# Kernel tuning notes

Measured on AMD Instinct MI355X. Metric: run time of the kernel, lower is better.

The kernel has to match this reference:

```python
import jax, jax.numpy as jnp
import numpy as np

N_NODES = 100000
N_EDGES = 1000000
IN_FEATS = 128
HID = 128
OUT_FEATS = 64


def _glorot(key, shape):
    fan_in, fan_out = shape
    lim = (6.0 / (fan_in + fan_out)) ** 0.5
    return jax.random.uniform(key, shape, jnp.float32, -lim, lim)


def setup_inputs() -> dict:
    key = jax.random.key(0)
    ks = jax.random.split(key, 12)
    x = jax.random.normal(ks[0], (N_NODES, IN_FEATS), jnp.float32)
    src = jax.random.randint(ks[1], (N_EDGES,), 0, N_NODES, jnp.int32)
    dst = jax.random.randint(ks[2], (N_EDGES,), 0, N_NODES, jnp.int32)
    return {
        "x": x, "src": src, "dst": dst,
        "w_self0": _glorot(ks[3], (IN_FEATS, HID)),
        "w_neigh0": _glorot(ks[4], (IN_FEATS, HID)),
        "b0": jnp.zeros((HID,), jnp.float32),
        "w_self1": _glorot(ks[5], (HID, HID)),
        "w_neigh1": _glorot(ks[6], (HID, HID)),
        "b1": jnp.zeros((HID,), jnp.float32),
        "w_self2": _glorot(ks[7], (HID, OUT_FEATS)),
        "w_neigh2": _glorot(ks[8], (HID, OUT_FEATS)),
        "b2": jnp.zeros((OUT_FEATS,), jnp.float32),
    }


def _sage_conv(x, src, dst, deg_inv, w_self, w_neigh, b):
    # irregular gather over neighbors, then mean segment-reduce onto dst
    neigh_sum = jax.ops.segment_sum(x[src], dst, num_segments=x.shape[0])  # [N, d]
    neigh_mean = neigh_sum * deg_inv  # zero-in-degree nodes -> 0
    return x @ w_self + neigh_mean @ w_neigh + b


def reference(x, src, dst,
              w_self0, w_neigh0, b0,
              w_self1, w_neigh1, b1,
              w_self2, w_neigh2, b2):
    n = x.shape[0]
    deg = jax.ops.segment_sum(jnp.ones_like(dst, jnp.float32), dst, num_segments=n)
    deg_inv = jnp.where(deg > 0, 1.0 / jnp.maximum(deg, 1.0), 0.0)[:, None]  # [N,1]
    h = _sage_conv(x, src, dst, deg_inv, w_self0, w_neigh0, b0)
    h = jax.nn.relu(h)  # dropout is identity in eval
    h = _sage_conv(h, src, dst, deg_inv, w_self1, w_neigh1, b1)
    h = jax.nn.relu(h)
    h = _sage_conv(h, src, dst, deg_inv, w_self2, w_neigh2, b2)
    return h
```

## Files before the change

kernel.cpp:

```cpp
#include <hip/hip_runtime.h>
#include <stdint.h>

#define N_NODES 100000
#define N_EDGES 1000000
#define NB 782
#define CAP 4096
#define EPB 2048
#define SCB ((N_EDGES + EPB - 1) / EPB)
#define PREPB 6442

typedef __attribute__((ext_vector_type(2))) _Float16 f16x2;
typedef __attribute__((ext_vector_type(8))) _Float16 f16x8;
typedef __attribute__((ext_vector_type(4))) float f32x4;

__device__ __forceinline__ unsigned short f2h(float f) {
  _Float16 h = (_Float16)f;
  return *(unsigned short*)&h;
}

__global__ void k_scatter_prep(const int* __restrict__ src, const int* __restrict__ dst,
                               int* __restrict__ bcnt, unsigned int* __restrict__ stage,
                               const float* __restrict__ x, unsigned short* __restrict__ xb,
                               const float* __restrict__ ws0, const float* __restrict__ wn0,
                               unsigned short* __restrict__ wt0,
                               const float* __restrict__ ws1, const float* __restrict__ wn1,
                               unsigned short* __restrict__ wt1,
                               const float* __restrict__ ws2, const float* __restrict__ wn2,
                               unsigned short* __restrict__ wt2) {
  __shared__ int h[NB];
  __shared__ int cur[NB];
  int t = threadIdx.x;
  if (blockIdx.x < SCB) {
    for (int i = t; i < NB; i += 256) h[i] = 0;
    __syncthreads();
    int base = blockIdx.x * EPB;
#pragma unroll 8
    for (int k = 0; k < EPB / 256; k++) {
      int i = base + t + k * 256;
      if (i < N_EDGES) atomicAdd(&h[dst[i] >> 7], 1);
    }
    __syncthreads();
    for (int i = t; i < NB; i += 256) {
      int c = h[i];
      cur[i] = c ? atomicAdd(&bcnt[i], c) : 0;
    }
    __syncthreads();
#pragma unroll 8
    for (int k = 0; k < EPB / 256; k++) {
      int i = base + t + k * 256;
      if (i < N_EDGES) {
        int d = dst[i];
        int b = d >> 7;
        int pos = atomicAdd(&cur[b], 1);
        stage[(size_t)b * CAP + pos] = ((unsigned int)(d & 127) << 17) | (unsigned int)src[i];
      }
    }
    return;
  }
  int b = blockIdx.x - SCB;
  if (b < 6250) {
    int i = b * 256 + t;
    float4 a = ((const float4*)x)[2 * i];
    float4 v = ((const float4*)x)[2 * i + 1];
    unsigned short r[8] = {f2h(a.x), f2h(a.y), f2h(a.z), f2h(a.w),
                           f2h(v.x), f2h(v.y), f2h(v.z), f2h(v.w)};
    *(uint4*)(xb + (size_t)i * 8) = *(uint4*)r;
    return;
  }
  int w = (b - 6250) * 256 + t;
  if (w < 16384) {
    int n = w >> 7, k = w & 127;
    wt0[n * 256 + k] = f2h(ws0[(size_t)k * 128 + n]);
    wt0[n * 256 + 128 + k] = f2h(wn0[(size_t)k * 128 + n]);
  } else if (w < 32768) {
    w -= 16384;
    int n = w >> 7, k = w & 127;
    wt1[n * 256 + k] = f2h(ws1[(size_t)k * 128 + n]);
    wt1[n * 256 + 128 + k] = f2h(wn1[(size_t)k * 128 + n]);
  } else {
    w -= 32768;
    int n = w >> 7, k = w & 127;
    float v = (n < 64) ? ws2[(size_t)k * 64 + n] : wn2[(size_t)k * 64 + (n - 64)];
    wt2[n * 128 + k] = f2h(v);
  }
}

__global__ void k_bucket(const unsigned int* __restrict__ stage, const int* __restrict__ bcnt,
                         int* __restrict__ csr, int* __restrict__ rowbeg,
                         int* __restrict__ rowend, float* __restrict__ dinv) {
  __shared__ int cnt[128], sc[128], cur[128];
  int b = blockIdx.x, t = threadIdx.x;
  int nb = bcnt[b];
  const unsigned int* sb = stage + (size_t)b * CAP;
  int e0 = b * CAP;
  if (t < 128) cnt[t] = 0;
  __syncthreads();
  for (int e = t; e < nb; e += 256)
    atomicAdd(&cnt[sb[e] >> 17], 1);
  __syncthreads();
  int myc = (t < 128) ? cnt[t] : 0;
  if (t < 128) sc[t] = myc;
  __syncthreads();
  for (int off = 1; off < 128; off <<= 1) {
    int a = (t < 128 && t >= off) ? sc[t - off] : 0;
    __syncthreads();
    if (t < 128) sc[t] += a;
    __syncthreads();
  }
  if (t < 128) {
    int node = b * 128 + t;
    int ex = sc[t] - myc;
    cur[t] = ex;
    if (node < N_NODES) {
      rowbeg[node] = e0 + ex;
      rowend[node] = e0 + ex + myc;
      dinv[node] = myc ? 1.0f / (float)myc : 0.0f;
    }
  }
  __syncthreads();
  for (int e = t; e < nb; e += 256) {
    unsigned int v = sb[e];
    int l = v >> 17;
    int pos = e0 + atomicAdd(&cur[l], 1);
    csr[pos] = (int)(v & 0x1FFFFu);
  }
}

__global__ void k_agg(const unsigned short* __restrict__ feat,
                      const int* __restrict__ rowbeg, const int* __restrict__ rowend,
                      const int* __restrict__ csr,
                      const float* __restrict__ dinv, unsigned short* __restrict__ nm) {
  int wv = threadIdx.x >> 6, lane = threadIdx.x & 63;
  int node = blockIdx.x * 4 + wv;
  if (node >= N_NODES) return;
  const uint4* fp = (const uint4*)feat;
  int s0 = rowbeg[node], s1 = rowend[node];
  int g = lane >> 4, c = lane & 15;
  f16x2 q0 = {0, 0}, q1 = {0, 0}, q2 = {0, 0}, q3 = {0, 0};
  for (int j = s0 + g; j < s1; j += 16) {
    int i1 = j + 4, i2 = j + 8, i3 = j + 12;
    bool h1 = i1 < s1, h2 = i2 < s1, h3 = i3 < s1;
    int c0 = csr[j];
    int c1 = h1 ? csr[i1] : 0;
    int c2 = h2 ? csr[i2] : 0;
    int c3 = h3 ? csr[i3] : 0;
    uint4 v0, v1, v2, v3;
    v0 = fp[(size_t)c0 * 16 + c];
    if (h1) v1 = fp[(size_t)c1 * 16 + c];
    if (h2) v2 = fp[(size_t)c2 * 16 + c];
    if (h3) v3 = fp[(size_t)c3 * 16 + c];
    q0 += *(const f16x2*)&v0.x; q1 += *(const f16x2*)&v0.y;
    q2 += *(const f16x2*)&v0.z; q3 += *(const f16x2*)&v0.w;
    if (h1) {
      q0 += *(const f16x2*)&v1.x; q1 += *(const f16x2*)&v1.y;
      q2 += *(const f16x2*)&v1.z; q3 += *(const f16x2*)&v1.w;
    }
    if (h2) {
      q0 += *(const f16x2*)&v2.x; q1 += *(const f16x2*)&v2.y;
      q2 += *(const f16x2*)&v2.z; q3 += *(const f16x2*)&v2.w;
    }
    if (h3) {
      q0 += *(const f16x2*)&v3.x; q1 += *(const f16x2*)&v3.y;
      q2 += *(const f16x2*)&v3.z; q3 += *(const f16x2*)&v3.w;
    }
  }
  float a0 = (float)q0[0], a1 = (float)q0[1], a2 = (float)q1[0], a3 = (float)q1[1];
  float a4 = (float)q2[0], a5 = (float)q2[1], a6 = (float)q3[0], a7 = (float)q3[1];
#define RED(x) x += __shfl_xor(x, 16); x += __shfl_xor(x, 32);
  RED(a0) RED(a1) RED(a2) RED(a3) RED(a4) RED(a5) RED(a6) RED(a7)
#undef RED
  if (g == 0) {
    float di = dinv[node];
    uint4 o;
    o.x = ((unsigned int)f2h(a1 * di) << 16) | (unsigned int)f2h(a0 * di);
    o.y = ((unsigned int)f2h(a3 * di) << 16) | (unsigned int)f2h(a2 * di);
    o.z = ((unsigned int)f2h(a5 * di) << 16) | (unsigned int)f2h(a4 * di);
    o.w = ((unsigned int)f2h(a7 * di) << 16) | (unsigned int)f2h(a6 * di);
    ((uint4*)(nm + (size_t)node * 128))[c] = o;
  }
}

__global__ void k_agg2(const unsigned short* __restrict__ zn,
                       const int* __restrict__ rowbeg, const int* __restrict__ rowend,
                       const int* __restrict__ csr, const float* __restrict__ dinv,
                       const float* __restrict__ self2, float* __restrict__ out) {
  int wv = threadIdx.x >> 6, lane = threadIdx.x & 63;
  int node = blockIdx.x * 4 + wv;
  if (node >= N_NODES) return;
  const uint4* fp = (const uint4*)zn;
  int s0 = rowbeg[node], s1 = rowend[node];
  int g = lane >> 3, c = lane & 7;
  f16x2 q0 = {0, 0}, q1 = {0, 0}, q2 = {0, 0}, q3 = {0, 0};
  for (int j = s0 + g; j < s1; j += 32) {
    int i1 = j + 8, i2 = j + 16, i3 = j + 24;
    bool h1 = i1 < s1, h2 = i2 < s1, h3 = i3 < s1;
    int c0 = csr[j];
    int c1 = h1 ? csr[i1] : 0;
    int c2 = h2 ? csr[i2] : 0;
    int c3 = h3 ? csr[i3] : 0;
    uint4 v0, v1, v2, v3;
    v0 = fp[(size_t)c0 * 8 + c];
    if (h1) v1 = fp[(size_t)c1 * 8 + c];
    if (h2) v2 = fp[(size_t)c2 * 8 + c];
    if (h3) v3 = fp[(size_t)c3 * 8 + c];
    q0 += *(const f16x2*)&v0.x; q1 += *(const f16x2*)&v0.y;
    q2 += *(const f16x2*)&v0.z; q3 += *(const f16x2*)&v0.w;
    if (h1) {
      q0 += *(const f16x2*)&v1.x; q1 += *(const f16x2*)&v1.y;
      q2 += *(const f16x2*)&v1.z; q3 += *(const f16x2*)&v1.w;
    }
    if (h2) {
      q0 += *(const f16x2*)&v2.x; q1 += *(const f16x2*)&v2.y;
      q2 += *(const f16x2*)&v2.z; q3 += *(const f16x2*)&v2.w;
    }
    if (h3) {
      q0 += *(const f16x2*)&v3.x; q1 += *(const f16x2*)&v3.y;
      q2 += *(const f16x2*)&v3.z; q3 += *(const f16x2*)&v3.w;
    }
  }
  float a0 = (float)q0[0], a1 = (float)q0[1], a2 = (float)q1[0], a3 = (float)q1[1];
  float a4 = (float)q2[0], a5 = (float)q2[1], a6 = (float)q3[0], a7 = (float)q3[1];
#define RED8(x) x += __shfl_xor(x, 8); x += __shfl_xor(x, 16); x += __shfl_xor(x, 32);
  RED8(a0) RED8(a1) RED8(a2) RED8(a3) RED8(a4) RED8(a5) RED8(a6) RED8(a7)
#undef RED8
  if (g == 0) {
    float di = dinv[node];
    const float4* sp = (const float4*)(self2 + (size_t)node * 64);
    float4 s0v = sp[c * 2], s1v = sp[c * 2 + 1];
    float4 o0 = {s0v.x + a0 * di, s0v.y + a1 * di, s0v.z + a2 * di, s0v.w + a3 * di};
    float4 o1 = {s1v.x + a4 * di, s1v.y + a5 * di, s1v.z + a6 * di, s1v.w + a7 * di};
    float4* op = (float4*)(out + (size_t)node * 64);
    op[c * 2] = o0;
    op[c * 2 + 1] = o1;
  }
}

template <int NOUT, bool RELU>
__global__ __launch_bounds__(256, 4) void k_mm(
    const unsigned short* __restrict__ A0, const unsigned short* __restrict__ A1,
    const unsigned short* __restrict__ WT, const float* __restrict__ Bv,
    unsigned short* __restrict__ OUT) {
  constexpr int NFC = NOUT / 64;
  __shared__ __align__(16) unsigned short sm[16896];
  const int row0 = blockIdx.x * 64;
  const int tid = threadIdx.x;

  for (int i = tid; i < 1024; i += 256) {
    int r = i >> 4, c = i & 15;
    int gr = row0 + r;
    if (gr >= N_NODES) gr = N_NODES - 1;
    *(uint4*)(sm + r * 264 + c * 8) = ((const uint4*)(A0 + (size_t)gr * 128))[c];
    *(uint4*)(sm + r * 264 + 128 + c * 8) = ((const uint4*)(A1 + (size_t)gr * 128))[c];
  }

  const int lane = tid & 63;
  const int w = tid >> 6;
  const int r16 = lane & 15;
  const int kg = lane >> 4;
  const int wc0 = w * (NOUT / 4);

  f32x4 acc[4][NFC];
#pragma unroll
  for (int rf = 0; rf < 4; rf++)
#pragma unroll
    for (int cf = 0; cf < NFC; cf++) acc[rf][cf] = (f32x4){0.f, 0.f, 0.f, 0.f};

  __syncthreads();

  const unsigned short* wtb = WT + (size_t)(wc0 + r16) * 256 + kg * 8;
  const unsigned short* asb = sm + r16 * 264 + kg * 8;

  for (int ks = 0; ks < 8; ks++) {
    f16x8 a[4];
#pragma unroll
    for (int rf = 0; rf < 4; rf++)
      a[rf] = *(const f16x8*)(asb + rf * 16 * 264 + ks * 32);
#pragma unroll
    for (int cf = 0; cf < NFC; cf++) {
      f16x8 b = *(const f16x8*)(wtb + cf * 16 * 256 + ks * 32);
#pragma unroll
      for (int rf = 0; rf < 4; rf++)
        acc[rf][cf] = __builtin_amdgcn_mfma_f32_16x16x32_f16(a[rf], b, acc[rf][cf], 0, 0, 0);
    }
  }

  __syncthreads();

  constexpr int LSO = NOUT + 8;
  unsigned short* so = sm;
#pragma unroll
  for (int rf = 0; rf < 4; rf++)
#pragma unroll
    for (int cf = 0; cf < NFC; cf++) {
      int col = wc0 + cf * 16 + r16;
      float bias = Bv[col];
#pragma unroll
      for (int r = 0; r < 4; r++) {
        int row = rf * 16 + kg * 4 + r;
        float v = acc[rf][cf][r] + bias;
        if (RELU) v = fmaxf(v, 0.f);
        so[row * LSO + col] = f2h(v);
      }
    }
  __syncthreads();
  for (int i = tid; i < 64 * (NOUT / 8); i += 256) {
    int r = i / (NOUT / 8), c = i % (NOUT / 8);
    int gr = row0 + r;
    if (gr < N_NODES)
      *(uint4*)(OUT + (size_t)gr * NOUT + c * 8) = *(const uint4*)(so + r * LSO + c * 8);
  }
}

__global__ __launch_bounds__(256, 4) void k_mm2(
    const unsigned short* __restrict__ A, const unsigned short* __restrict__ WT,
    const float* __restrict__ Bv, float* __restrict__ SELF,
    unsigned short* __restrict__ ZN) {
  __shared__ __align__(16) unsigned short sm[64 * 136];
  const int row0 = blockIdx.x * 64;
  const int tid = threadIdx.x;

  for (int i = tid; i < 1024; i += 256) {
    int r = i >> 4, c = i & 15;
    int gr = row0 + r;
    if (gr >= N_NODES) gr = N_NODES - 1;
    *(uint4*)(sm + r * 136 + c * 8) = ((const uint4*)(A + (size_t)gr * 128))[c];
  }

  const int lane = tid & 63;
  const int w = tid >> 6;
  const int r16 = lane & 15;
  const int kg = lane >> 4;
  const int wc0 = w * 32;

  f32x4 acc[4][2];
#pragma unroll
  for (int rf = 0; rf < 4; rf++)
#pragma unroll
    for (int cf = 0; cf < 2; cf++) acc[rf][cf] = (f32x4){0.f, 0.f, 0.f, 0.f};

  __syncthreads();

  const unsigned short* wtb = WT + (size_t)(wc0 + r16) * 128 + kg * 8;
  const unsigned short* asb = sm + r16 * 136 + kg * 8;

  for (int ks = 0; ks < 4; ks++) {
    f16x8 a[4];
#pragma unroll
    for (int rf = 0; rf < 4; rf++)
      a[rf] = *(const f16x8*)(asb + rf * 16 * 136 + ks * 32);
#pragma unroll
    for (int cf = 0; cf < 2; cf++) {
      f16x8 b = *(const f16x8*)(wtb + cf * 16 * 128 + ks * 32);
#pragma unroll
      for (int rf = 0; rf < 4; rf++)
        acc[rf][cf] = __builtin_amdgcn_mfma_f32_16x16x32_f16(a[rf], b, acc[rf][cf], 0, 0, 0);
    }
  }

  __syncthreads();

  float* sof = (float*)sm;
#pragma unroll
  for (int rf = 0; rf < 4; rf++)
#pragma unroll
    for (int cf = 0; cf < 2; cf++) {
      int col = wc0 + cf * 16 + r16;
      if (col < 64) {
        float bias = Bv[col];
#pragma unroll
        for (int r = 0; r < 4; r++) {
          int row = rf * 16 + kg * 4 + r;
          sof[row * 68 + col] = acc[rf][cf][r] + bias;
        }
      }
    }
  __syncthreads();
  for (int i = tid; i < 1024; i += 256) {
    int r = i >> 4, c = i & 15;
    int gr = row0 + r;
    if (gr < N_NODES)
      *(float4*)(SELF + (size_t)gr * 64 + c * 4) = *(const float4*)(sof + r * 68 + c * 4);
  }
  __syncthreads();

  unsigned short* soh = sm;
#pragma unroll
  for (int rf = 0; rf < 4; rf++)
#pragma unroll
    for (int cf = 0; cf < 2; cf++) {
      int col = wc0 + cf * 16 + r16;
      if (col >= 64) {
#pragma unroll
        for (int r = 0; r < 4; r++) {
          int row = rf * 16 + kg * 4 + r;
          soh[row * 72 + (col - 64)] = f2h(acc[rf][cf][r]);
        }
      }
    }
  __syncthreads();
  for (int i = tid; i < 512; i += 256) {
    int r = i >> 3, c = i & 7;
    int gr = row0 + r;
    if (gr < N_NODES)
      *(uint4*)(ZN + (size_t)gr * 64 + c * 8) = *(const uint4*)(soh + r * 72 + c * 8);
  }
}


extern "C" void kernel_launch(void* const* d_in, const int* in_sizes, int n_in,
                              void* d_out, int out_size, void* d_ws, size_t ws_size,
                              hipStream_t stream) {
  const float* x   = (const float*)d_in[0];
  const int*   src = (const int*)d_in[1];
  const int*   dst = (const int*)d_in[2];
  const float* ws0 = (const float*)d_in[3];
  const float* wn0 = (const float*)d_in[4];
  const float* b0  = (const float*)d_in[5];
  const float* ws1 = (const float*)d_in[6];
  const float* wn1 = (const float*)d_in[7];
  const float* b1  = (const float*)d_in[8];
  const float* ws2 = (const float*)d_in[9];
  const float* wn2 = (const float*)d_in[10];
  const float* b2  = (const float*)d_in[11];
  float* out = (float*)d_out;

  uint8_t* base = (uint8_t*)d_ws;
  size_t off = 0;
  auto alloc = [&](size_t bytes) -> void* {
    void* p = base + off;
    off = (off + bytes + 255) & ~(size_t)255;
    return p;
  };
  int*   rowbeg  = (int*)alloc((size_t)N_NODES * 4);
  int*   rowend  = (int*)alloc((size_t)N_NODES * 4);
  float* dinv    = (float*)alloc((size_t)N_NODES * 4);
  int*   csr     = (int*)alloc((size_t)NB * CAP * 4);
  unsigned int* stage = (unsigned int*)alloc((size_t)NB * CAP * 4);
  int*   bcnt    = (int*)alloc((size_t)NB * 4);
  unsigned short* xb  = (unsigned short*)alloc((size_t)N_NODES * 128 * 2);
  unsigned short* nmb = (unsigned short*)alloc((size_t)N_NODES * 128 * 2);
  unsigned short* h1b = (unsigned short*)alloc((size_t)N_NODES * 128 * 2);
  unsigned short* h2b = (unsigned short*)alloc((size_t)N_NODES * 128 * 2);
  float* self2 = (float*)alloc((size_t)N_NODES * 64 * 4);
  unsigned short* znb = (unsigned short*)alloc((size_t)N_NODES * 64 * 2);
  unsigned short* wt0 = (unsigned short*)alloc(128 * 256 * 2);
  unsigned short* wt1 = (unsigned short*)alloc(128 * 256 * 2);
  unsigned short* wt2 = (unsigned short*)alloc(128 * 128 * 2);

  hipMemsetAsync(bcnt, 0, (size_t)NB * 4, stream);
  k_scatter_prep<<<SCB + PREPB, 256, 0, stream>>>(src, dst, bcnt, stage,
                                                  x, xb, ws0, wn0, wt0,
                                                  ws1, wn1, wt1, ws2, wn2, wt2);
  k_bucket<<<NB, 256, 0, stream>>>(stage, bcnt, csr, rowbeg, rowend, dinv);

  const int GMM = (N_NODES + 63) / 64;

  k_agg<<<25000, 256, 0, stream>>>(xb, rowbeg, rowend, csr, dinv, nmb);
  k_mm<128, true><<<GMM, 256, 0, stream>>>(xb, nmb, wt0, b0, h1b);
  k_agg<<<25000, 256, 0, stream>>>(h1b, rowbeg, rowend, csr, dinv, nmb);
  k_mm<128, true><<<GMM, 256, 0, stream>>>(h1b, nmb, wt1, b1, h2b);
  k_mm2<<<GMM, 256, 0, stream>>>(h2b, wt2, b2, self2, znb);
  k_agg2<<<25000, 256, 0, stream>>>(znb, rowbeg, rowend, csr, dinv, self2, out);
}
```

Baseline: 238.5 us.

## Replace global-atomic bucket scatter with count/scan/scatter passes and enlarge aggregation blocks

```diff
diff --git a/kernel.cpp b/kernel.cpp
--- a/kernel.cpp
+++ b/kernel.cpp
@@ -4,7 +4,7 @@
 #define N_NODES 100000
 #define N_EDGES 1000000
 #define NB 782
-#define CAP 4096
+#define CAP 2048
 #define EPB 2048
 #define SCB ((N_EDGES + EPB - 1) / EPB)
 #define PREPB 6442
@@ -18,17 +18,15 @@
   return *(unsigned short*)&h;
 }
 
-__global__ void k_scatter_prep(const int* __restrict__ src, const int* __restrict__ dst,
-                               int* __restrict__ bcnt, unsigned int* __restrict__ stage,
-                               const float* __restrict__ x, unsigned short* __restrict__ xb,
-                               const float* __restrict__ ws0, const float* __restrict__ wn0,
-                               unsigned short* __restrict__ wt0,
-                               const float* __restrict__ ws1, const float* __restrict__ wn1,
-                               unsigned short* __restrict__ wt1,
-                               const float* __restrict__ ws2, const float* __restrict__ wn2,
-                               unsigned short* __restrict__ wt2) {
+__global__ void k_count_prep(const int* __restrict__ dst, int* __restrict__ hcnt,
+                             const float* __restrict__ x, unsigned short* __restrict__ xb,
+                             const float* __restrict__ ws0, const float* __restrict__ wn0,
+                             unsigned short* __restrict__ wt0,
+                             const float* __restrict__ ws1, const float* __restrict__ wn1,
+                             unsigned short* __restrict__ wt1,
+                             const float* __restrict__ ws2, const float* __restrict__ wn2,
+                             unsigned short* __restrict__ wt2) {
   __shared__ int h[NB];
-  __shared__ int cur[NB];
   int t = threadIdx.x;
   if (blockIdx.x < SCB) {
     for (int i = t; i < NB; i += 256) h[i] = 0;
@@ -40,21 +38,8 @@
       if (i < N_EDGES) atomicAdd(&h[dst[i] >> 7], 1);
     }
     __syncthreads();
-    for (int i = t; i < NB; i += 256) {
-      int c = h[i];
-      cur[i] = c ? atomicAdd(&bcnt[i], c) : 0;
-    }
-    __syncthreads();
-#pragma unroll 8
-    for (int k = 0; k < EPB / 256; k++) {
-      int i = base + t + k * 256;
-      if (i < N_EDGES) {
-        int d = dst[i];
-        int b = d >> 7;
-        int pos = atomicAdd(&cur[b], 1);
-        stage[(size_t)b * CAP + pos] = ((unsigned int)(d & 127) << 17) | (unsigned int)src[i];
-      }
-    }
+    int* hrow = hcnt + (size_t)blockIdx.x * NB;
+    for (int i = t; i < NB; i += 256) hrow[i] = h[i];
     return;
   }
   int b = blockIdx.x - SCB;
@@ -85,6 +70,44 @@
   }
 }
 
+__global__ __launch_bounds__(512) void k_hscan(const int* __restrict__ hcnt,
+                                               int* __restrict__ hoff,
+                                               int* __restrict__ bcnt) {
+  __shared__ int sc[512];
+  int bucket = blockIdx.x, t = threadIdx.x;
+  int v = (t < SCB) ? hcnt[(size_t)t * NB + bucket] : 0;
+  sc[t] = v;
+  __syncthreads();
+  for (int off = 1; off < 512; off <<= 1) {
+    int a = (t >= off) ? sc[t - off] : 0;
+    __syncthreads();
+    sc[t] += a;
+    __syncthreads();
+  }
+  hoff[(size_t)bucket * 512 + t] = sc[t] - v;
+  if (t == 511) bcnt[bucket] = sc[511];
+}
+
+__global__ void k_scatter(const int* __restrict__ src, const int* __restrict__ dst,
+                          const int* __restrict__ hoff, unsigned int* __restrict__ stage) {
+  __shared__ int cur[NB];
+  int t = threadIdx.x;
+  int blk = blockIdx.x;
+  for (int i = t; i < NB; i += 256) cur[i] = hoff[(size_t)i * 512 + blk];
+  __syncthreads();
+  int base = blk * EPB;
+#pragma unroll 8
+  for (int k = 0; k < EPB / 256; k++) {
+    int i = base + t + k * 256;
+    if (i < N_EDGES) {
+      int d = dst[i];
+      int b = d >> 7;
+      int pos = atomicAdd(&cur[b], 1);
+      stage[(size_t)b * CAP + pos] = ((unsigned int)(d & 127) << 17) | (unsigned int)src[i];
+    }
+  }
+}
+
 __global__ void k_bucket(const unsigned int* __restrict__ stage, const int* __restrict__ bcnt,
                          int* __restrict__ csr, int* __restrict__ rowbeg,
                          int* __restrict__ rowend, float* __restrict__ dinv) {
@@ -126,12 +149,13 @@
   }
 }
 
-__global__ void k_agg(const unsigned short* __restrict__ feat,
-                      const int* __restrict__ rowbeg, const int* __restrict__ rowend,
-                      const int* __restrict__ csr,
-                      const float* __restrict__ dinv, unsigned short* __restrict__ nm) {
+__global__ __launch_bounds__(1024) void k_agg(
+    const unsigned short* __restrict__ feat,
+    const int* __restrict__ rowbeg, const int* __restrict__ rowend,
+    const int* __restrict__ csr,
+    const float* __restrict__ dinv, unsigned short* __restrict__ nm) {
   int wv = threadIdx.x >> 6, lane = threadIdx.x & 63;
-  int node = blockIdx.x * 4 + wv;
+  int node = blockIdx.x * 16 + wv;
   if (node >= N_NODES) return;
   const uint4* fp = (const uint4*)feat;
   int s0 = rowbeg[node], s1 = rowend[node];
@@ -180,12 +204,13 @@
   }
 }
 
-__global__ void k_agg2(const unsigned short* __restrict__ zn,
-                       const int* __restrict__ rowbeg, const int* __restrict__ rowend,
-                       const int* __restrict__ csr, const float* __restrict__ dinv,
-                       const float* __restrict__ self2, float* __restrict__ out) {
+__global__ __launch_bounds__(1024) void k_agg2(
+    const unsigned short* __restrict__ zn,
+    const int* __restrict__ rowbeg, const int* __restrict__ rowend,
+    const int* __restrict__ csr, const float* __restrict__ dinv,
+    const float* __restrict__ self2, float* __restrict__ out) {
   int wv = threadIdx.x >> 6, lane = threadIdx.x & 63;
-  int node = blockIdx.x * 4 + wv;
+  int node = blockIdx.x * 16 + wv;
   if (node >= N_NODES) return;
   const uint4* fp = (const uint4*)zn;
   int s0 = rowbeg[node], s1 = rowend[node];
@@ -436,6 +461,8 @@
   float* dinv    = (float*)alloc((size_t)N_NODES * 4);
   int*   csr     = (int*)alloc((size_t)NB * CAP * 4);
   unsigned int* stage = (unsigned int*)alloc((size_t)NB * CAP * 4);
+  int*   hcnt    = (int*)alloc((size_t)512 * NB * 4);
+  int*   hoff    = (int*)alloc((size_t)NB * 512 * 4);
   int*   bcnt    = (int*)alloc((size_t)NB * 4);
   unsigned short* xb  = (unsigned short*)alloc((size_t)N_NODES * 128 * 2);
   unsigned short* nmb = (unsigned short*)alloc((size_t)N_NODES * 128 * 2);
@@ -447,18 +474,19 @@
   unsigned short* wt1 = (unsigned short*)alloc(128 * 256 * 2);
   unsigned short* wt2 = (unsigned short*)alloc(128 * 128 * 2);
 
-  hipMemsetAsync(bcnt, 0, (size_t)NB * 4, stream);
-  k_scatter_prep<<<SCB + PREPB, 256, 0, stream>>>(src, dst, bcnt, stage,
-                                                  x, xb, ws0, wn0, wt0,
-                                                  ws1, wn1, wt1, ws2, wn2, wt2);
+  k_count_prep<<<SCB + PREPB, 256, 0, stream>>>(dst, hcnt, x, xb, ws0, wn0, wt0,
+                                                ws1, wn1, wt1, ws2, wn2, wt2);
+  k_hscan<<<NB, 512, 0, stream>>>(hcnt, hoff, bcnt);
+  k_scatter<<<SCB, 256, 0, stream>>>(src, dst, hoff, stage);
   k_bucket<<<NB, 256, 0, stream>>>(stage, bcnt, csr, rowbeg, rowend, dinv);
 
   const int GMM = (N_NODES + 63) / 64;
-
-  k_agg<<<25000, 256, 0, stream>>>(xb, rowbeg, rowend, csr, dinv, nmb);
+  const int GAGG = N_NODES / 16;
+
+  k_agg<<<GAGG, 1024, 0, stream>>>(xb, rowbeg, rowend, csr, dinv, nmb);
   k_mm<128, true><<<GMM, 256, 0, stream>>>(xb, nmb, wt0, b0, h1b);
-  k_agg<<<25000, 256, 0, stream>>>(h1b, rowbeg, rowend, csr, dinv, nmb);
+  k_agg<<<GAGG, 1024, 0, stream>>>(h1b, rowbeg, rowend, csr, dinv, nmb);
   k_mm<128, true><<<GMM, 256, 0, stream>>>(h1b, nmb, wt1, b1, h2b);
   k_mm2<<<GMM, 256, 0, stream>>>(h2b, wt2, b2, self2, znb);
-  k_agg2<<<25000, 256, 0, stream>>>(znb, rowbeg, rowend, csr, dinv, self2, out);
-}
+  k_agg2<<<GAGG, 1024, 0, stream>>>(znb, rowbeg, rowend, csr, dinv, self2, out);
+}
```

Measured after the change: 245.3 us. 2.9% more time.
